# Optimization experiments

Measured on AMD Instinct MI355X. Metric: run time of the kernel, lower is better.

Reference implementation:

```python
import jax, jax.numpy as jnp
import numpy as np

KS = 4          # kernel_size per pseudo-dim (open linear B-splines, degree 1)
GRID = 28       # level-0 grid side
BATCH = 256     # number of graphs
NUM_FIRST_FC = 49


def _grid(n, B):
    """Batched 8-neighborhood grid graph with 2D pseudo-coords in [0,1]."""
    rs, cs = np.meshgrid(np.arange(n), np.arange(n), indexing='ij')
    idx = rs * n + cs
    src_l, dst_l, ps_l = [], [], []
    for dr in (-1, 0, 1):
        for dc in (-1, 0, 1):
            if dr == 0 and dc == 0:
                continue
            r2, c2 = rs + dr, cs + dc
            ok = (r2 >= 0) & (r2 < n) & (c2 >= 0) & (c2 < n)
            src_l.append(idx[ok])
            dst_l.append((r2 * n + c2)[ok])
            m = int(ok.sum())
            ps_l.append(np.stack([np.full(m, (dr + 1) / 2.0),
                                  np.full(m, (dc + 1) / 2.0)], 1))
    src = np.concatenate(src_l)
    dst = np.concatenate(dst_l)
    pseudo = np.concatenate(ps_l).astype(np.float32)
    off = (np.arange(B) * n * n)[:, None]
    src_b = (src[None] + off).reshape(-1)
    dst_b = (dst[None] + off).reshape(-1)
    return (np.stack([src_b, dst_b]).astype(np.int32),
            np.tile(pseudo, (B, 1)))


def _cluster(n, B):
    """Factor-4 (2x2 block) graclus-style cluster assignment, batched."""
    rs, cs = np.meshgrid(np.arange(n), np.arange(n), indexing='ij')
    c = ((rs // 2) * (n // 2) + (cs // 2)).reshape(-1)
    off = (np.arange(B) * (n // 2) ** 2)[:, None]
    return (c[None] + off).reshape(-1).astype(np.int32)


def setup_inputs() -> dict:
    key = jax.random.key(0)
    ks = jax.random.split(key, 16)
    e0, p0 = _grid(GRID, BATCH)          # 28x28 level
    e1, p1 = _grid(GRID // 2, BATCH)     # 14x14 level
    c0 = _cluster(GRID, BATCH)           # 784 -> 196 per graph
    c1 = _cluster(GRID // 2, BATCH)      # 196 -> 49 per graph
    N0 = BATCH * GRID * GRID
    s = 0.1
    inp = {
        'x': jax.random.normal(ks[0], (N0, 1), jnp.float32),
        'edge_index0': jnp.asarray(e0), 'pseudo0': jnp.asarray(p0),
        'edge_index1': jnp.asarray(e1), 'pseudo1': jnp.asarray(p1),
        'cluster0': jnp.asarray(c0), 'cluster1': jnp.asarray(c1),
        'W1': s * jax.random.normal(ks[1], (16, 1, 32), jnp.float32),
        'root1': s * jax.random.normal(ks[2], (1, 32), jnp.float32),
        'b1': jnp.zeros((32,), jnp.float32),
        'W2': s * jax.random.normal(ks[3], (16, 32, 32), jnp.float32),
        'root2': s * jax.random.normal(ks[4], (32, 32), jnp.float32),
        'b2': jnp.zeros((32,), jnp.float32),
        'W3': s * jax.random.normal(ks[5], (16, 32, 64), jnp.float32),
        'root3': s * jax.random.normal(ks[6], (32, 64), jnp.float32),
        'b3': jnp.zeros((64,), jnp.float32),
        'W4': s * jax.random.normal(ks[7], (16, 64, 64), jnp.float32),
        'root4': s * jax.random.normal(ks[8], (64, 64), jnp.float32),
        'b4': jnp.zeros((64,), jnp.float32),
        'fc1_W': s * jax.random.normal(ks[9], (NUM_FIRST_FC * 64, 512), jnp.float32),
        'fc1_b': jnp.zeros((512,), jnp.float32),
        'fc2_W': s * jax.random.normal(ks[10], (512, 10), jnp.float32),
        'fc2_b': jnp.zeros((10,), jnp.float32),
    }
    return inp


def spline_conv(x, src, dst, pseudo, W, root, bias):
    """SplineGCN layer: degree-1 open B-spline weighting over 2D pseudo-coords,
    mean aggregation over incoming edges, plus root weight and bias."""
    n = x.shape[0]
    pos = pseudo * (KS - 1)                       # [E,2] in [0, KS-1]
    i0f = jnp.clip(jnp.floor(pos), 0, KS - 2)
    frac = pos - i0f                              # [E,2]
    i0 = i0f.astype(jnp.int32)
    XW = jnp.einsum('ni,kio->kno', x, W)          # [K, N, out]: per-kernel transform
    msg = jnp.zeros((src.shape[0], W.shape[2]), x.dtype)
    for a in (0, 1):
        wa = frac[:, 0] if a else 1.0 - frac[:, 0]
        for b in (0, 1):
            wb = frac[:, 1] if b else 1.0 - frac[:, 1]
            k = (i0[:, 0] + a) * KS + (i0[:, 1] + b)     # flat kernel index [E]
            msg = msg + (wa * wb)[:, None] * XW[k, src]  # gather per-edge
    agg = jax.ops.segment_sum(msg, dst, num_segments=n)
    deg = jax.ops.segment_sum(jnp.ones_like(dst, dtype=x.dtype), dst,
                              num_segments=n)
    return agg / jnp.maximum(deg, 1.0)[:, None] + x @ root + bias


def pool4(x, cluster):
    # GraclusMaxPool(2): two halving levels == factor-4 cluster max-pool
    return jax.ops.segment_max(x, cluster, num_segments=x.shape[0] // 4)


def reference(x, edge_index0, pseudo0, edge_index1, pseudo1, cluster0, cluster1,
              W1, root1, b1, W2, root2, b2, W3, root3, b3, W4, root4, b4,
              fc1_W, fc1_b, fc2_W, fc2_b):
    s0, d0 = edge_index0[0], edge_index0[1]
    s1, d1 = edge_index1[0], edge_index1[1]
    h = jax.nn.elu(spline_conv(x, s0, d0, pseudo0, W1, root1, b1))
    h = jax.nn.elu(spline_conv(h, s0, d0, pseudo0, W2, root2, b2))
    h = pool4(h, cluster0)
    h = jax.nn.elu(spline_conv(h, s1, d1, pseudo1, W3, root3, b3))
    h = jax.nn.elu(spline_conv(h, s1, d1, pseudo1, W4, root4, b4))
    h = pool4(h, cluster1)
    h = h.reshape(-1, NUM_FIRST_FC * 64)           # [B, 49*64]
    h = jax.nn.elu(h @ fc1_W + fc1_b)
    # dropout is identity in eval / deterministic reference
    logits = h @ fc2_W + fc2_b
    return jax.nn.log_softmax(logits, axis=-1)
```

## Files before the change

kernel.cpp:

```cpp
#include <hip/hip_runtime.h>

typedef unsigned short u16;
typedef short bf16x8 __attribute__((ext_vector_type(8)));
typedef float f32x4 __attribute__((ext_vector_type(4)));

__device__ __constant__ const int DRS[8] = {-1,-1,-1, 0, 0, 1, 1, 1};
__device__ __constant__ const int DCS[8] = {-1, 0, 1,-1, 1,-1, 0, 1};

__device__ inline float bf2f(u16 u) { return __uint_as_float(((unsigned)u) << 16); }
__device__ inline u16 f2bf(float f) {
  unsigned u = __float_as_uint(f);
  return (u16)((u + 0x7fffu + ((u >> 16) & 1u)) >> 16);
}
__device__ inline float eluf(float v) { return v > 0.f ? v : (__expf(v) - 1.f); }
__device__ inline unsigned pk2(float a, float b) {
  return (unsigned)f2bf(a) | ((unsigned)f2bf(b) << 16);
}

__device__ inline float weff_val(const float* __restrict__ W, int d, int off, int stride) {
  int dd = d >= 4 ? d + 1 : d;
  int dr = dd / 3 - 1, dc = dd - (dd / 3) * 3 - 1;
  int kr0, kr1, nr; float wr0, wr1;
  if (dr < 0)       { kr0 = 0; wr0 = 1.f; kr1 = 0; wr1 = 0.f; nr = 1; }
  else if (dr == 0) { kr0 = 1; wr0 = .5f; kr1 = 2; wr1 = .5f; nr = 2; }
  else              { kr0 = 3; wr0 = 1.f; kr1 = 0; wr1 = 0.f; nr = 1; }
  int kc0, kc1, nc; float wc0, wc1;
  if (dc < 0)       { kc0 = 0; wc0 = 1.f; kc1 = 0; wc1 = 0.f; nc = 1; }
  else if (dc == 0) { kc0 = 1; wc0 = .5f; kc1 = 2; wc1 = .5f; nc = 2; }
  else              { kc0 = 3; wc0 = 1.f; kc1 = 0; wc1 = 0.f; nc = 1; }
  float acc = wr0 * wc0 * W[(kr0 * 4 + kc0) * stride + off];
  if (nc == 2) acc += wr0 * wc1 * W[(kr0 * 4 + kc1) * stride + off];
  if (nr == 2) {
    acc += wr1 * wc0 * W[(kr1 * 4 + kc0) * stride + off];
    if (nc == 2) acc += wr1 * wc1 * W[(kr1 * 4 + kc1) * stride + off];
  }
  return acc;
}

__device__ inline int kperm32(int p) { return (p >> 1) + ((p & 1) << 4); }

__global__ __launch_bounds__(256) void pack_all(
    const float* __restrict__ W1,
    const float* __restrict__ W2, const float* __restrict__ rt2,
    const float* __restrict__ W3, const float* __restrict__ rt3,
    const float* __restrict__ W4, const float* __restrict__ rt4,
    const float* __restrict__ fcW,
    float* __restrict__ wf1, u16* __restrict__ wp2,
    u16* __restrict__ wp3, u16* __restrict__ wp4, u16* __restrict__ wfc) {
  __shared__ u16 T[32 * 514];
  int blk = blockIdx.x, t = threadIdx.x;
  if (blk < 98) {
    int q = blk;
#pragma unroll
    for (int i = 0; i < 16; ++i) {
      int idx = i * 1024 + t * 4;
      int k = idx >> 9, n = idx & 511;
      float4 v = *reinterpret_cast<const float4*>(fcW + (size_t)(q * 32 + k) * 512 + n);
      T[k * 514 + n]     = f2bf(v.x);
      T[k * 514 + n + 1] = f2bf(v.y);
      T[k * 514 + n + 2] = f2bf(v.z);
      T[k * 514 + n + 3] = f2bf(v.w);
    }
    __syncthreads();
#pragma unroll
    for (int w = 0; w < 8; ++w) {
      int g = w * 256 + t;
      int nt = g >> 6, l = g & 63;
      union { int4 q4; u16 s[8]; } R;
#pragma unroll
      for (int j = 0; j < 8; ++j)
        R.s[j] = T[((l >> 4) * 8 + j) * 514 + nt * 16 + (l & 15)];
      *reinterpret_cast<int4*>(wfc + ((size_t)(q * 32 + nt) * 64 + l) * 8) = R.q4;
    }
    return;
  }
  int idx = (blk - 98) * 256 + t;
  if (idx < 256) {
    int d = idx >> 5, o = idx & 31;
    wf1[idx] = weff_val(W1, d, o, 32);
    return;
  }
  if (idx < 9472) {
    int local = idx - 256;
    int j = local & 7, l = (local >> 3) & 63, chunk = local >> 9;
    int ct = chunk & 1, tap = chunk >> 1;
    int k = (l >> 4) * 8 + j, n = ct * 16 + (l & 15);
    float v = tap < 8 ? weff_val(W2, tap, k * 32 + n, 1024) : rt2[k * 32 + n];
    wp2[local] = f2bf(v);
    return;
  }
  if (idx < 27904) {
    int local = idx - 9472;
    int j = local & 7, l = (local >> 3) & 63, chunk = local >> 9;
    int ct = chunk & 3, tap = chunk >> 2;
    int k = kperm32((l >> 4) * 8 + j), n = ct * 16 + (l & 15);
    float v = tap < 8 ? weff_val(W3, tap, k * 64 + n, 2048) : rt3[k * 64 + n];
    wp3[local] = f2bf(v);
    return;
  }
  if (idx < 64768) {
    int local = idx - 27904;
    int j = local & 7, l = (local >> 3) & 63, chunk = local >> 9;
    int q = chunk & 1, tmp = chunk >> 1;
    int ct = tmp & 3, tap = tmp >> 2;
    int k = q * 32 + kperm32((l >> 4) * 8 + j), n = ct * 16 + (l & 15);
    float v = tap < 8 ? weff_val(W4, tap, k * 64 + n, 4096) : rt4[k * 64 + n];
    wp4[local] = f2bf(v);
  }
}

__global__ __launch_bounds__(1024, 4) void conv_mega(
    const float* __restrict__ x,
    const float* __restrict__ wf1, const float* __restrict__ rt1, const float* __restrict__ b1,
    const u16* __restrict__ wp2, const float* __restrict__ b2,
    const u16* __restrict__ wp3, const float* __restrict__ b3,
    const u16* __restrict__ wp4, const float* __restrict__ b4,
    u16* __restrict__ A6) {
  extern __shared__ char smem[];
  int4* H1 = (int4*)smem;
  int4* H3 = (int4*)smem;
  u16*  H5 = (u16*)(smem + 17408);
  int4* H4 = (int4*)(smem + 42496);
  unsigned* H4u = (unsigned*)(smem + 42496);
  float* XT = (float*)(smem + 61568);
  int4*     H2 = (int4*)(smem + 75520);
  unsigned* H2u = (unsigned*)(smem + 75520);

  int img = blockIdx.x, tid = threadIdx.x;
  int lane = tid & 63, wid = tid >> 6;
  int kcb = lane >> 4, n0 = lane & 15;
  int4 z4 = make_int4(0, 0, 0, 0);
  f32x4 zz = {0.f, 0.f, 0.f, 0.f};

  for (int i = tid; i < 3848; i += 1024) H1[i] = z4;
  if (tid < 960) {
    int r = tid >> 5, c = tid & 31;
    bool in = (r >= 1) && (r <= 28) && (c >= 1) && (c <= 28);
    XT[tid] = in ? x[(size_t)img * 784 + (r - 1) * 28 + (c - 1)] : 0.f;
  }
  __syncthreads();

  if (tid < 784) {
    int px = tid;
    int r = px / 28, c = px - 28 * (px / 28);
    float acc[32];
#pragma unroll
    for (int o = 0; o < 32; ++o) acc[o] = 0.f;
#pragma unroll
    for (int d = 0; d < 8; ++d) {
      float xv = XT[(r + 1 - DRS[d]) * 32 + (c + 1 - DCS[d])];
#pragma unroll
      for (int o = 0; o < 32; ++o) acc[o] = fmaf(xv, wf1[d * 32 + o], acc[o]);
    }
    float inv = 1.f / (float)((3 - (r == 0) - (r == 27)) * (3 - (c == 0) - (c == 27)) - 1);
    float xc = XT[(r + 1) * 32 + c + 1];
    unsigned pk[16];
#pragma unroll
    for (int h = 0; h < 16; ++h)
      pk[h] = pk2(eluf(acc[2 * h] * inv + xc * rt1[2 * h] + b1[2 * h]),
                  eluf(acc[2 * h + 1] * inv + xc * rt1[2 * h + 1] + b1[2 * h + 1]));
#pragma unroll
    for (int kc = 0; kc < 4; ++kc)
      H1[kc * 962 + (r + 1) * 32 + (c + 1)] =
          make_int4(pk[4 * kc], pk[4 * kc + 1], pk[4 * kc + 2], pk[4 * kc + 3]);
  }
  __syncthreads();

  {
    bf16x8 w2[9][2];
#pragma unroll
    for (int tap = 0; tap < 9; ++tap)
#pragma unroll
      for (int ct = 0; ct < 2; ++ct)
        w2[tap][ct] = *(const bf16x8*)(wp2 + (tap * 2 + ct) * 512 + lane * 8);
    for (int t = wid; t < 49; t += 16) {
      int pxm = t * 16 + n0;
      int r = pxm / 28, c = pxm - 28 * (pxm / 28);
      f32x4 an[2] = {zz, zz}, ar[2] = {zz, zz};
#pragma unroll
      for (int d = 0; d < 8; ++d) {
        bf16x8 a = *(const bf16x8*)&H1[kcb * 962 + (r + 1 - DRS[d]) * 32 + (c + 1 - DCS[d])];
        an[0] = __builtin_amdgcn_mfma_f32_16x16x32_bf16(a, w2[d][0], an[0], 0, 0, 0);
        an[1] = __builtin_amdgcn_mfma_f32_16x16x32_bf16(a, w2[d][1], an[1], 0, 0, 0);
      }
      {
        bf16x8 a = *(const bf16x8*)&H1[kcb * 962 + (r + 1) * 32 + (c + 1)];
        ar[0] = __builtin_amdgcn_mfma_f32_16x16x32_bf16(a, w2[8][0], ar[0], 0, 0, 0);
        ar[1] = __builtin_amdgcn_mfma_f32_16x16x32_bf16(a, w2[8][1], ar[1], 0, 0, 0);
      }
#pragma unroll
      for (int j = 0; j < 4; ++j) {
        int pm = t * 16 + (lane >> 4) * 4 + j;
        int rm = pm / 28, cm = pm - 28 * (pm / 28);
        float inv = 1.f / (float)((3 - (rm == 0) - (rm == 27)) * (3 - (cm == 0) - (cm == 27)) - 1);
        H2u[pm * 16 + n0] = pk2(eluf(an[0][j] * inv + ar[0][j] + b2[n0]),
                                eluf(an[1][j] * inv + ar[1][j] + b2[16 + n0]));
      }
    }
  }
  __syncthreads();

  for (int i = tid; i < 1032; i += 1024) {
    int kc = i & 3, rem = i >> 2;
    int4 v = z4;
    if (rem < 256) {
      int pr = rem >> 4, pc = rem & 15;
      if (pr >= 1 && pr <= 14 && pc >= 1 && pc <= 14) {
        int px0 = (2 * (pr - 1)) * 28 + 2 * (pc - 1);
        union { int4 q; u16 s[8]; } A, B, C, D, R;
        A.q = H2[px0 * 4 + kc]; B.q = H2[(px0 + 1) * 4 + kc];
        C.q = H2[(px0 + 28) * 4 + kc]; D.q = H2[(px0 + 29) * 4 + kc];
#pragma unroll
        for (int e = 0; e < 8; ++e)
          R.s[e] = f2bf(fmaxf(fmaxf(bf2f(A.s[e]), bf2f(B.s[e])),
                              fmaxf(bf2f(C.s[e]), bf2f(D.s[e]))));
        v = R.q;
      }
    }
    H3[kc * 258 + rem] = v;
  }
  for (int i = tid; i < 2064; i += 1024) H4[i] = z4;
  __syncthreads();

  {
    int ct0 = wid & 1, t0 = wid >> 1;
    bf16x8 w3[9][2];
#pragma unroll
    for (int tap = 0; tap < 9; ++tap)
#pragma unroll
      for (int cc = 0; cc < 2; ++cc)
        w3[tap][cc] = *(const bf16x8*)(wp3 + (tap * 4 + ct0 * 2 + cc) * 512 + lane * 8);
    for (int t = t0; t < 13; t += 8) {
      int pxm = t * 16 + n0; if (pxm > 195) pxm = 195;
      int r = pxm / 14, c = pxm - 14 * (pxm / 14);
      f32x4 an[2] = {zz, zz}, ar[2] = {zz, zz};
#pragma unroll
      for (int d = 0; d < 8; ++d) {
        bf16x8 a = *(const bf16x8*)&H3[kcb * 258 + (r + 1 - DRS[d]) * 16 + (c + 1 - DCS[d])];
        an[0] = __builtin_amdgcn_mfma_f32_16x16x32_bf16(a, w3[d][0], an[0], 0, 0, 0);
        an[1] = __builtin_amdgcn_mfma_f32_16x16x32_bf16(a, w3[d][1], an[1], 0, 0, 0);
      }
      {
        bf16x8 a = *(const bf16x8*)&H3[kcb * 258 + (r + 1) * 16 + (c + 1)];
        ar[0] = __builtin_amdgcn_mfma_f32_16x16x32_bf16(a, w3[8][0], ar[0], 0, 0, 0);
        ar[1] = __builtin_amdgcn_mfma_f32_16x16x32_bf16(a, w3[8][1], ar[1], 0, 0, 0);
      }
#pragma unroll
      for (int j = 0; j < 4; ++j) {
        int pm = t * 16 + (lane >> 4) * 4 + j;
        if (pm < 196) {
          int rm = pm / 14, cm = pm - 14 * (pm / 14);
          float inv = 1.f / (float)((3 - (rm == 0) - (rm == 13)) * (3 - (cm == 0) - (cm == 13)) - 1);
          unsigned v = pk2(eluf(an[0][j] * inv + ar[0][j] + b3[ct0 * 32 + n0]),
                           eluf(an[1][j] * inv + ar[1][j] + b3[ct0 * 32 + 16 + n0]));
          H4u[((ct0 * 4 + (n0 >> 2)) * 258 + (rm + 1) * 16 + (cm + 1)) * 4 + (n0 & 3)] = v;
        }
      }
    }
  }
  __syncthreads();

  {
    int ctg = wid & 3, t0 = wid >> 2;
    bf16x8 w4[9][2];
#pragma unroll
    for (int tap = 0; tap < 9; ++tap)
#pragma unroll
      for (int kq = 0; kq < 2; ++kq)
        w4[tap][kq] = *(const bf16x8*)(wp4 + ((tap * 4 + ctg) * 2 + kq) * 512 + lane * 8);
    for (int t = t0; t < 13; t += 4) {
      int pxm = t * 16 + n0; if (pxm > 195) pxm = 195;
      int r = pxm / 14, c = pxm - 14 * (pxm / 14);
      f32x4 an = zz, ar = zz;
#pragma unroll
      for (int d = 0; d < 8; ++d) {
        int rr = r + 1 - DRS[d], c2 = c + 1 - DCS[d];
#pragma unroll
        for (int kq = 0; kq < 2; ++kq) {
          bf16x8 a = *(const bf16x8*)&H4[(kq * 4 + kcb) * 258 + rr * 16 + c2];
          an = __builtin_amdgcn_mfma_f32_16x16x32_bf16(a, w4[d][kq], an, 0, 0, 0);
        }
      }
#pragma unroll
      for (int kq = 0; kq < 2; ++kq) {
        bf16x8 a = *(const bf16x8*)&H4[(kq * 4 + kcb) * 258 + (r + 1) * 16 + (c + 1)];
        ar = __builtin_amdgcn_mfma_f32_16x16x32_bf16(a, w4[8][kq], ar, 0, 0, 0);
      }
#pragma unroll
      for (int j = 0; j < 4; ++j) {
        int pm = t * 16 + (lane >> 4) * 4 + j;
        if (pm < 196) {
          int rm = pm / 14, cm = pm - 14 * (pm / 14);
          float inv = 1.f / (float)((3 - (rm == 0) - (rm == 13)) * (3 - (cm == 0) - (cm == 13)) - 1);
          int n = ctg * 16 + n0;
          H5[pm * 64 + n] = f2bf(eluf(an[j] * inv + ar[j] + b4[n]));
        }
      }
    }
  }
  __syncthreads();

  if (tid < 392) {
    int kc = tid & 7, q = tid >> 3;
    int r2 = q / 7, c2 = q - 7 * (q / 7);
    int px0 = (2 * r2) * 14 + 2 * c2;
    union { int4 q4; u16 s[8]; } A, B, C, D, R;
    A.q4 = *(const int4*)&H5[px0 * 64 + kc * 8];
    B.q4 = *(const int4*)&H5[(px0 + 1) * 64 + kc * 8];
    C.q4 = *(const int4*)&H5[(px0 + 14) * 64 + kc * 8];
    D.q4 = *(const int4*)&H5[(px0 + 15) * 64 + kc * 8];
#pragma unroll
    for (int e = 0; e < 8; ++e)
      R.s[e] = f2bf(fmaxf(fmaxf(bf2f(A.s[e]), bf2f(B.s[e])),
                          fmaxf(bf2f(C.s[e]), bf2f(D.s[e]))));
    *(int4*)(A6 + ((size_t)img * 49 + q) * 64 + kc * 8) = R.q4;
  }
}

__global__ __launch_bounds__(128) void fc1_mfma(
    const u16* __restrict__ A6, const u16* __restrict__ wfc,
    const float* __restrict__ fc1b, u16* __restrict__ h) {
  int blk = blockIdx.x;
  int mt = blk & 15, bn = blk >> 4;
  int lane = threadIdx.x & 63, w = threadIdx.x >> 6;
  int NT = bn * 2 + w;
  f32x4 acc0 = {0.f, 0.f, 0.f, 0.f}, acc1 = {0.f, 0.f, 0.f, 0.f};
  const u16* Ab = A6 + (size_t)(mt * 16 + (lane & 15)) * 3136 + (lane >> 4) * 8;
  const u16* Bb = wfc + (size_t)NT * 512 + (size_t)lane * 8;
#pragma unroll 7
  for (int qq = 0; qq < 98; qq += 2) {
    bf16x8 a0 = *(const bf16x8*)(Ab + qq * 32);
    bf16x8 b0 = *(const bf16x8*)(Bb + (size_t)qq * 16384);
    acc0 = __builtin_amdgcn_mfma_f32_16x16x32_bf16(a0, b0, acc0, 0, 0, 0);
    bf16x8 a1 = *(const bf16x8*)(Ab + qq * 32 + 32);
    bf16x8 b1 = *(const bf16x8*)(Bb + (size_t)qq * 16384 + 16384);
    acc1 = __builtin_amdgcn_mfma_f32_16x16x32_bf16(a1, b1, acc1, 0, 0, 0);
  }
#pragma unroll
  for (int j = 0; j < 4; ++j) {
    int row = mt * 16 + (lane >> 4) * 4 + j;
    int col = NT * 16 + (lane & 15);
    float v = acc0[j] + acc1[j] + fc1b[col];
    h[(size_t)row * 512 + col] = f2bf(eluf(v));
  }
}

__global__ __launch_bounds__(64) void fc2_kernel(
    const u16* __restrict__ h, const float* __restrict__ W,
    const float* __restrict__ bias, float* __restrict__ out) {
  int bb = blockIdx.x;
  int t = threadIdx.x;
  float acc[10];
#pragma unroll
  for (int o = 0; o < 10; ++o) acc[o] = 0.f;
  bf16x8 hv = *(const bf16x8*)(h + (size_t)bb * 512 + t * 8);
#pragma unroll
  for (int kk = 0; kk < 8; ++kk) {
    float xv = bf2f((u16)hv[kk]);
    int k = t * 8 + kk;
#pragma unroll
    for (int o = 0; o < 10; ++o) acc[o] = fmaf(xv, W[k * 10 + o], acc[o]);
  }
#pragma unroll
  for (int o = 0; o < 10; ++o) {
    float v = acc[o];
#pragma unroll
    for (int s = 32; s >= 1; s >>= 1) v += __shfl_xor(v, s);
    acc[o] = v + bias[o];
  }
  float m = acc[0];
#pragma unroll
  for (int o = 1; o < 10; ++o) m = fmaxf(m, acc[o]);
  float sum = 0.f;
#pragma unroll
  for (int o = 0; o < 10; ++o) sum += __expf(acc[o] - m);
  float lse = m + __logf(sum);
  if (t < 10) out[bb * 10 + t] = acc[t] - lse;
}

extern "C" void kernel_launch(void* const* d_in, const int* in_sizes, int n_in,
                              void* d_out, int out_size, void* d_ws, size_t ws_size,
                              hipStream_t stream) {
  const float* x    = (const float*)d_in[0];
  const float* W1   = (const float*)d_in[7];
  const float* r1   = (const float*)d_in[8];
  const float* b1   = (const float*)d_in[9];
  const float* W2   = (const float*)d_in[10];
  const float* r2   = (const float*)d_in[11];
  const float* b2   = (const float*)d_in[12];
  const float* W3   = (const float*)d_in[13];
  const float* r3   = (const float*)d_in[14];
  const float* b3   = (const float*)d_in[15];
  const float* W4   = (const float*)d_in[16];
  const float* r4   = (const float*)d_in[17];
  const float* b4   = (const float*)d_in[18];
  const float* fc1W = (const float*)d_in[19];
  const float* fc1b = (const float*)d_in[20];
  const float* fc2W = (const float*)d_in[21];
  const float* fc2b = (const float*)d_in[22];

  char* wsb = (char*)d_ws;
  float* wf1  = (float*)(wsb + 0);
  u16*   wp2  = (u16*)(wsb + 1024);
  u16*   wp3  = (u16*)(wsb + 19456);
  u16*   wp4  = (u16*)(wsb + 56320);
  u16*   wfc  = (u16*)(wsb + 130048);
  u16*   A6   = (u16*)(wsb + 3341312);
  u16*   hbuf = (u16*)(wsb + 4946944);

  pack_all<<<351, 256, 0, stream>>>(W1, W2, r2, W3, r3, W4, r4, fc1W,
                                    wf1, wp2, wp3, wp4, wfc);

  (void)hipFuncSetAttribute((const void*)conv_mega,
                            hipFuncAttributeMaxDynamicSharedMemorySize, 125696);
  conv_mega<<<256, 1024, 125696, stream>>>(x, wf1, r1, b1, wp2, b2, wp3, b3,
                                           wp4, b4, A6);

  fc1_mfma<<<256, 128, 0, stream>>>(A6, wfc, fc1b, hbuf);
  fc2_kernel<<<256, 64, 0, stream>>>(hbuf, fc2W, fc2b, (float*)d_out);
}
```

Measured before the change: 53.08 us.

## Split fused conv kernel into half-image level-0 kernel and level-1 kernel

Splits the single per-image conv_mega kernel into two launches. convA processes each image's 28x28 level in two 14-row halves, recomputing a one-row halo, and writes the pooled 14x14 features to global memory. convB reads that buffer and runs the level-1 convolutions. The goal is to use 512 smaller blocks with less shared memory, raising occupancy and CU coverage for the heavy level-0 stage. The cost is an extra launch, a global round trip for the pooled activations, and redundant halo computation.

Measured after the change: 56.05 us. +5.6%, slower.

```diff
diff --git a/kernel.cpp b/kernel.cpp
--- a/kernel.cpp
+++ b/kernel.cpp
@@ -109,22 +109,124 @@
   }
 }
 
-__global__ __launch_bounds__(1024, 4) void conv_mega(
+__global__ __launch_bounds__(512, 4) void convA(
     const float* __restrict__ x,
     const float* __restrict__ wf1, const float* __restrict__ rt1, const float* __restrict__ b1,
     const u16* __restrict__ wp2, const float* __restrict__ b2,
+    u16* __restrict__ A3) {
+  extern __shared__ char smem[];
+  int4*     H1  = (int4*)smem;
+  float*    XT  = (float*)(smem + 32896);
+  unsigned* H2u = (unsigned*)(smem + 35200);
+  int4*     H2q = (int4*)(smem + 35200);
+
+  int blk = blockIdx.x, tid = threadIdx.x;
+  int img = blk >> 1, half = blk & 1;
+  int base_r = half * 14;
+  int lane = tid & 63, wid = tid >> 6;
+  int kcb = lane >> 4, n0 = lane & 15;
+  int4 z4 = make_int4(0, 0, 0, 0);
+  f32x4 zz = {0.f, 0.f, 0.f, 0.f};
+
+  for (int i = tid; i < 2056; i += 512) H1[i] = z4;
+  for (int i = tid; i < 576; i += 512) {
+    int r = i >> 5, c = i & 31;
+    int gr = base_r - 2 + r, gc = c - 1;
+    bool in = (gr >= 0) && (gr < 28) && (gc >= 0) && (gc < 28);
+    XT[i] = in ? x[(size_t)img * 784 + gr * 28 + gc] : 0.f;
+  }
+  __syncthreads();
+
+  if (tid < 448) {
+    int lr = tid / 28, c = tid - 28 * (tid / 28);
+    int gr = base_r - 1 + lr;
+    if (gr >= 0 && gr < 28) {
+      float acc[32];
+#pragma unroll
+      for (int o = 0; o < 32; ++o) acc[o] = 0.f;
+#pragma unroll
+      for (int d = 0; d < 8; ++d) {
+        float xv = XT[(lr + 1 - DRS[d]) * 32 + (c + 1 - DCS[d])];
+#pragma unroll
+        for (int o = 0; o < 32; ++o) acc[o] = fmaf(xv, wf1[d * 32 + o], acc[o]);
+      }
+      float inv = 1.f / (float)((3 - (gr == 0) - (gr == 27)) * (3 - (c == 0) - (c == 27)) - 1);
+      float xc = XT[(lr + 1) * 32 + c + 1];
+      unsigned pk[16];
+#pragma unroll
+      for (int h = 0; h < 16; ++h)
+        pk[h] = pk2(eluf(acc[2 * h] * inv + xc * rt1[2 * h] + b1[2 * h]),
+                    eluf(acc[2 * h + 1] * inv + xc * rt1[2 * h + 1] + b1[2 * h + 1]));
+#pragma unroll
+      for (int kc = 0; kc < 4; ++kc)
+        H1[kc * 514 + lr * 32 + (c + 1)] =
+            make_int4(pk[4 * kc], pk[4 * kc + 1], pk[4 * kc + 2], pk[4 * kc + 3]);
+    }
+  }
+  __syncthreads();
+
+  {
+    bf16x8 w2[9][2];
+#pragma unroll
+    for (int tap = 0; tap < 9; ++tap)
+#pragma unroll
+      for (int ct = 0; ct < 2; ++ct)
+        w2[tap][ct] = *(const bf16x8*)(wp2 + (tap * 2 + ct) * 512 + lane * 8);
+    for (int t = wid; t < 25; t += 8) {
+      int pxm = t * 16 + n0; if (pxm > 391) pxm = 391;
+      int lr2 = pxm / 28, c = pxm - 28 * (pxm / 28);
+      f32x4 an[2] = {zz, zz}, ar[2] = {zz, zz};
+#pragma unroll
+      for (int d = 0; d < 8; ++d) {
+        bf16x8 a = *(const bf16x8*)&H1[kcb * 514 + (lr2 + 1 - DRS[d]) * 32 + (c + 1 - DCS[d])];
+        an[0] = __builtin_amdgcn_mfma_f32_16x16x32_bf16(a, w2[d][0], an[0], 0, 0, 0);
+        an[1] = __builtin_amdgcn_mfma_f32_16x16x32_bf16(a, w2[d][1], an[1], 0, 0, 0);
+      }
+      {
+        bf16x8 a = *(const bf16x8*)&H1[kcb * 514 + (lr2 + 1) * 32 + (c + 1)];
+        ar[0] = __builtin_amdgcn_mfma_f32_16x16x32_bf16(a, w2[8][0], ar[0], 0, 0, 0);
+        ar[1] = __builtin_amdgcn_mfma_f32_16x16x32_bf16(a, w2[8][1], ar[1], 0, 0, 0);
+      }
+#pragma unroll
+      for (int j = 0; j < 4; ++j) {
+        int pm = t * 16 + (lane >> 4) * 4 + j;
+        if (pm < 392) {
+          int rmg = base_r + pm / 28, cm = pm - 28 * (pm / 28);
+          float inv = 1.f / (float)((3 - (rmg == 0) - (rmg == 27)) * (3 - (cm == 0) - (cm == 27)) - 1);
+          H2u[pm * 16 + n0] = pk2(eluf(an[0][j] * inv + ar[0][j] + b2[n0]),
+                                  eluf(an[1][j] * inv + ar[1][j] + b2[16 + n0]));
+        }
+      }
+    }
+  }
+  __syncthreads();
+
+  if (tid < 392) {
+    int kc = tid & 3, q = tid >> 2;
+    int orl = q / 14, oc = q - 14 * (q / 14);
+    int p0 = (2 * orl) * 28 + 2 * oc;
+    union { int4 q4; u16 s[8]; } A, B, C, D, R;
+    A.q4 = H2q[p0 * 4 + kc];        B.q4 = H2q[(p0 + 1) * 4 + kc];
+    C.q4 = H2q[(p0 + 28) * 4 + kc]; D.q4 = H2q[(p0 + 29) * 4 + kc];
+#pragma unroll
+    for (int e = 0; e < 8; ++e)
+      R.s[e] = f2bf(fmaxf(fmaxf(bf2f(A.s[e]), bf2f(B.s[e])),
+                          fmaxf(bf2f(C.s[e]), bf2f(D.s[e]))));
+    int qg = (half * 7 + orl) * 14 + oc;
+    *(int4*)(A3 + ((size_t)img * 196 + qg) * 32 + kc * 8) = R.q4;
+  }
+}
+
+__global__ __launch_bounds__(1024, 4) void convB(
+    const u16* __restrict__ A3,
     const u16* __restrict__ wp3, const float* __restrict__ b3,
     const u16* __restrict__ wp4, const float* __restrict__ b4,
     u16* __restrict__ A6) {
   extern __shared__ char smem[];
-  int4* H1 = (int4*)smem;
-  int4* H3 = (int4*)smem;
-  u16*  H5 = (u16*)(smem + 17408);
-  int4* H4 = (int4*)(smem + 42496);
+  int4*     H3  = (int4*)smem;
+  u16*      H5  = (u16*)(smem + 17408);
+  int4*     H4  = (int4*)(smem + 42496);
   unsigned* H4u = (unsigned*)(smem + 42496);
-  float* XT = (float*)(smem + 61568);
-  int4*     H2 = (int4*)(smem + 75520);
-  unsigned* H2u = (unsigned*)(smem + 75520);
 
   int img = blockIdx.x, tid = threadIdx.x;
   int lane = tid & 63, wid = tid >> 6;
@@ -132,92 +234,15 @@
   int4 z4 = make_int4(0, 0, 0, 0);
   f32x4 zz = {0.f, 0.f, 0.f, 0.f};
 
-  for (int i = tid; i < 3848; i += 1024) H1[i] = z4;
-  if (tid < 960) {
-    int r = tid >> 5, c = tid & 31;
-    bool in = (r >= 1) && (r <= 28) && (c >= 1) && (c <= 28);
-    XT[tid] = in ? x[(size_t)img * 784 + (r - 1) * 28 + (c - 1)] : 0.f;
-  }
-  __syncthreads();
-
-  if (tid < 784) {
-    int px = tid;
-    int r = px / 28, c = px - 28 * (px / 28);
-    float acc[32];
-#pragma unroll
-    for (int o = 0; o < 32; ++o) acc[o] = 0.f;
-#pragma unroll
-    for (int d = 0; d < 8; ++d) {
-      float xv = XT[(r + 1 - DRS[d]) * 32 + (c + 1 - DCS[d])];
-#pragma unroll
-      for (int o = 0; o < 32; ++o) acc[o] = fmaf(xv, wf1[d * 32 + o], acc[o]);
-    }
-    float inv = 1.f / (float)((3 - (r == 0) - (r == 27)) * (3 - (c == 0) - (c == 27)) - 1);
-    float xc = XT[(r + 1) * 32 + c + 1];
-    unsigned pk[16];
-#pragma unroll
-    for (int h = 0; h < 16; ++h)
-      pk[h] = pk2(eluf(acc[2 * h] * inv + xc * rt1[2 * h] + b1[2 * h]),
-                  eluf(acc[2 * h + 1] * inv + xc * rt1[2 * h + 1] + b1[2 * h + 1]));
-#pragma unroll
-    for (int kc = 0; kc < 4; ++kc)
-      H1[kc * 962 + (r + 1) * 32 + (c + 1)] =
-          make_int4(pk[4 * kc], pk[4 * kc + 1], pk[4 * kc + 2], pk[4 * kc + 3]);
-  }
-  __syncthreads();
-
-  {
-    bf16x8 w2[9][2];
-#pragma unroll
-    for (int tap = 0; tap < 9; ++tap)
-#pragma unroll
-      for (int ct = 0; ct < 2; ++ct)
-        w2[tap][ct] = *(const bf16x8*)(wp2 + (tap * 2 + ct) * 512 + lane * 8);
-    for (int t = wid; t < 49; t += 16) {
-      int pxm = t * 16 + n0;
-      int r = pxm / 28, c = pxm - 28 * (pxm / 28);
-      f32x4 an[2] = {zz, zz}, ar[2] = {zz, zz};
-#pragma unroll
-      for (int d = 0; d < 8; ++d) {
-        bf16x8 a = *(const bf16x8*)&H1[kcb * 962 + (r + 1 - DRS[d]) * 32 + (c + 1 - DCS[d])];
-        an[0] = __builtin_amdgcn_mfma_f32_16x16x32_bf16(a, w2[d][0], an[0], 0, 0, 0);
-        an[1] = __builtin_amdgcn_mfma_f32_16x16x32_bf16(a, w2[d][1], an[1], 0, 0, 0);
-      }
-      {
-        bf16x8 a = *(const bf16x8*)&H1[kcb * 962 + (r + 1) * 32 + (c + 1)];
-        ar[0] = __builtin_amdgcn_mfma_f32_16x16x32_bf16(a, w2[8][0], ar[0], 0, 0, 0);
-        ar[1] = __builtin_amdgcn_mfma_f32_16x16x32_bf16(a, w2[8][1], ar[1], 0, 0, 0);
-      }
-#pragma unroll
-      for (int j = 0; j < 4; ++j) {
-        int pm = t * 16 + (lane >> 4) * 4 + j;
-        int rm = pm / 28, cm = pm - 28 * (pm / 28);
-        float inv = 1.f / (float)((3 - (rm == 0) - (rm == 27)) * (3 - (cm == 0) - (cm == 27)) - 1);
-        H2u[pm * 16 + n0] = pk2(eluf(an[0][j] * inv + ar[0][j] + b2[n0]),
-                                eluf(an[1][j] * inv + ar[1][j] + b2[16 + n0]));
-      }
-    }
-  }
-  __syncthreads();
-
   for (int i = tid; i < 1032; i += 1024) {
     int kc = i & 3, rem = i >> 2;
     int4 v = z4;
     if (rem < 256) {
       int pr = rem >> 4, pc = rem & 15;
-      if (pr >= 1 && pr <= 14 && pc >= 1 && pc <= 14) {
-        int px0 = (2 * (pr - 1)) * 28 + 2 * (pc - 1);
-        union { int4 q; u16 s[8]; } A, B, C, D, R;
-        A.q = H2[px0 * 4 + kc]; B.q = H2[(px0 + 1) * 4 + kc];
-        C.q = H2[(px0 + 28) * 4 + kc]; D.q = H2[(px0 + 29) * 4 + kc];
-#pragma unroll
-        for (int e = 0; e < 8; ++e)
-          R.s[e] = f2bf(fmaxf(fmaxf(bf2f(A.s[e]), bf2f(B.s[e])),
-                              fmaxf(bf2f(C.s[e]), bf2f(D.s[e]))));
-        v = R.q;
-      }
-    }
-    H3[kc * 258 + rem] = v;
+      if (pr >= 1 && pr <= 14 && pc >= 1 && pc <= 14)
+        v = *(const int4*)(A3 + ((size_t)img * 196 + (pr - 1) * 14 + (pc - 1)) * 32 + kc * 8);
+    }
+    if ((i & 3) == kc) H3[kc * 258 + rem] = v;
   }
   for (int i = tid; i < 2064; i += 1024) H4[i] = z4;
   __syncthreads();
@@ -407,14 +432,16 @@
   u16*   wfc  = (u16*)(wsb + 130048);
   u16*   A6   = (u16*)(wsb + 3341312);
   u16*   hbuf = (u16*)(wsb + 4946944);
+  u16*   A3   = (u16*)(wsb + 5209088);
 
   pack_all<<<351, 256, 0, stream>>>(W1, W2, r2, W3, r3, W4, r4, fc1W,
                                     wf1, wp2, wp3, wp4, wfc);
 
-  (void)hipFuncSetAttribute((const void*)conv_mega,
-                            hipFuncAttributeMaxDynamicSharedMemorySize, 125696);
-  conv_mega<<<256, 1024, 125696, stream>>>(x, wf1, r1, b1, wp2, b2, wp3, b3,
-                                           wp4, b4, A6);
+  convA<<<512, 512, 60288, stream>>>(x, wf1, r1, b1, wp2, b2, A3);
+
+  (void)hipFuncSetAttribute((const void*)convB,
+                            hipFuncAttributeMaxDynamicSharedMemorySize, 75520);
+  convB<<<256, 1024, 75520, stream>>>(A3, wp3, b3, wp4, b4, A6);
 
   fc1_mfma<<<256, 128, 0, stream>>>(A6, wfc, fc1b, hbuf);
   fc2_kernel<<<256, 64, 0, stream>>>(hbuf, fc2W, fc2b, (float*)d_out);
```

## Split fc1 K-reduction across four waves and widen conv4 per-wave output tiles

Applied to the files above, without the earlier changes.

The fc1 kernel now runs 512 threads per block. Each block splits the 98-step K loop into four chunks handled by separate waves, and the partial MFMA accumulators are reduced through shared memory. This raises parallelism and the number of memory loads in flight for the bandwidth-bound weight stream. In the conv4 stage, each wave now computes two 16-column output tiles and loads weights from global memory inside the loop instead of preloading them into registers, which cuts register pressure but adds repeated weight loads.

New measurement: 70.04 us. +31.9%, slower.

```diff
diff --git a/kernel.cpp b/kernel.cpp
--- a/kernel.cpp
+++ b/kernel.cpp
@@ -261,30 +261,30 @@
   __syncthreads();
 
   {
-    int ctg = wid & 3, t0 = wid >> 2;
-    bf16x8 w4[9][2];
-#pragma unroll
-    for (int tap = 0; tap < 9; ++tap)
-#pragma unroll
-      for (int kq = 0; kq < 2; ++kq)
-        w4[tap][kq] = *(const bf16x8*)(wp4 + ((tap * 4 + ctg) * 2 + kq) * 512 + lane * 8);
-    for (int t = t0; t < 13; t += 4) {
+    int ct0 = wid & 1, t0 = wid >> 1;
+    for (int t = t0; t < 13; t += 8) {
       int pxm = t * 16 + n0; if (pxm > 195) pxm = 195;
       int r = pxm / 14, c = pxm - 14 * (pxm / 14);
-      f32x4 an = zz, ar = zz;
+      f32x4 an[2] = {zz, zz}, ar[2] = {zz, zz};
 #pragma unroll
       for (int d = 0; d < 8; ++d) {
         int rr = r + 1 - DRS[d], c2 = c + 1 - DCS[d];
 #pragma unroll
         for (int kq = 0; kq < 2; ++kq) {
           bf16x8 a = *(const bf16x8*)&H4[(kq * 4 + kcb) * 258 + rr * 16 + c2];
-          an = __builtin_amdgcn_mfma_f32_16x16x32_bf16(a, w4[d][kq], an, 0, 0, 0);
+          bf16x8 w0 = *(const bf16x8*)(wp4 + ((size_t)((d * 4 + ct0 * 2) * 2 + kq) * 64 + lane) * 8);
+          bf16x8 w1 = *(const bf16x8*)(wp4 + ((size_t)((d * 4 + ct0 * 2 + 1) * 2 + kq) * 64 + lane) * 8);
+          an[0] = __builtin_amdgcn_mfma_f32_16x16x32_bf16(a, w0, an[0], 0, 0, 0);
+          an[1] = __builtin_amdgcn_mfma_f32_16x16x32_bf16(a, w1, an[1], 0, 0, 0);
         }
       }
 #pragma unroll
       for (int kq = 0; kq < 2; ++kq) {
         bf16x8 a = *(const bf16x8*)&H4[(kq * 4 + kcb) * 258 + (r + 1) * 16 + (c + 1)];
-        ar = __builtin_amdgcn_mfma_f32_16x16x32_bf16(a, w4[8][kq], ar, 0, 0, 0);
+        bf16x8 w0 = *(const bf16x8*)(wp4 + ((size_t)((8 * 4 + ct0 * 2) * 2 + kq) * 64 + lane) * 8);
+        bf16x8 w1 = *(const bf16x8*)(wp4 + ((size_t)((8 * 4 + ct0 * 2 + 1) * 2 + kq) * 64 + lane) * 8);
+        ar[0] = __builtin_amdgcn_mfma_f32_16x16x32_bf16(a, w0, ar[0], 0, 0, 0);
+        ar[1] = __builtin_amdgcn_mfma_f32_16x16x32_bf16(a, w1, ar[1], 0, 0, 0);
       }
 #pragma unroll
       for (int j = 0; j < 4; ++j) {
@@ -292,8 +292,9 @@
         if (pm < 196) {
           int rm = pm / 14, cm = pm - 14 * (pm / 14);
           float inv = 1.f / (float)((3 - (rm == 0) - (rm == 13)) * (3 - (cm == 0) - (cm == 13)) - 1);
-          int n = ctg * 16 + n0;
-          H5[pm * 64 + n] = f2bf(eluf(an[j] * inv + ar[j] + b4[n]));
+          int na = ct0 * 32 + n0, nb = ct0 * 32 + 16 + n0;
+          H5[pm * 64 + na] = f2bf(eluf(an[0][j] * inv + ar[0][j] + b4[na]));
+          H5[pm * 64 + nb] = f2bf(eluf(an[1][j] * inv + ar[1][j] + b4[nb]));
         }
       }
     }
@@ -317,31 +318,41 @@
   }
 }
 
-__global__ __launch_bounds__(128) void fc1_mfma(
+__global__ __launch_bounds__(512) void fc1_mfma(
     const u16* __restrict__ A6, const u16* __restrict__ wfc,
     const float* __restrict__ fc1b, u16* __restrict__ h) {
+  __shared__ f32x4 red[8][64];
   int blk = blockIdx.x;
-  int mt = blk & 15, bn = blk >> 4;
-  int lane = threadIdx.x & 63, w = threadIdx.x >> 6;
-  int NT = bn * 2 + w;
-  f32x4 acc0 = {0.f, 0.f, 0.f, 0.f}, acc1 = {0.f, 0.f, 0.f, 0.f};
+  int mt = blk & 15, nt2 = blk >> 4;
+  int lane = threadIdx.x & 63, wid = threadIdx.x >> 6;
+  int half = wid & 1, ks = wid >> 1;
+  int NT = nt2 * 2 + half;
+  const int q0 = ks * 25 - ((ks >= 3) ? 1 : 0);
+  const int q1 = (ks + 1) * 25 - ((ks >= 2) ? 1 : 0);
+  f32x4 acc = {0.f, 0.f, 0.f, 0.f};
   const u16* Ab = A6 + (size_t)(mt * 16 + (lane & 15)) * 3136 + (lane >> 4) * 8;
-  const u16* Bb = wfc + (size_t)NT * 512 + (size_t)lane * 8;
-#pragma unroll 7
-  for (int qq = 0; qq < 98; qq += 2) {
-    bf16x8 a0 = *(const bf16x8*)(Ab + qq * 32);
-    bf16x8 b0 = *(const bf16x8*)(Bb + (size_t)qq * 16384);
-    acc0 = __builtin_amdgcn_mfma_f32_16x16x32_bf16(a0, b0, acc0, 0, 0, 0);
-    bf16x8 a1 = *(const bf16x8*)(Ab + qq * 32 + 32);
-    bf16x8 b1 = *(const bf16x8*)(Bb + (size_t)qq * 16384 + 16384);
-    acc1 = __builtin_amdgcn_mfma_f32_16x16x32_bf16(a1, b1, acc1, 0, 0, 0);
-  }
-#pragma unroll
-  for (int j = 0; j < 4; ++j) {
-    int row = mt * 16 + (lane >> 4) * 4 + j;
-    int col = NT * 16 + (lane & 15);
-    float v = acc0[j] + acc1[j] + fc1b[col];
-    h[(size_t)row * 512 + col] = f2bf(eluf(v));
+  for (int qq = q0; qq < q1; ++qq) {
+    bf16x8 a = *(const bf16x8*)(Ab + qq * 32);
+    bf16x8 b = *(const bf16x8*)(wfc + ((size_t)(qq * 32 + NT) * 64 + lane) * 8);
+    acc = __builtin_amdgcn_mfma_f32_16x16x32_bf16(a, b, acc, 0, 0, 0);
+  }
+  red[wid][lane] = acc;
+  __syncthreads();
+  if (wid < 2) {
+    f32x4 s = red[wid][lane];
+#pragma unroll
+    for (int k2 = 1; k2 < 4; ++k2) {
+      f32x4 p = red[k2 * 2 + wid][lane];
+#pragma unroll
+      for (int j = 0; j < 4; ++j) s[j] += p[j];
+    }
+    int NTo = nt2 * 2 + wid;
+#pragma unroll
+    for (int j = 0; j < 4; ++j) {
+      int row = mt * 16 + (lane >> 4) * 4 + j;
+      int col = NTo * 16 + (lane & 15);
+      h[(size_t)row * 512 + col] = f2bf(eluf(s[j] + fc1b[col]));
+    }
   }
 }
 
@@ -416,6 +427,6 @@
   conv_mega<<<256, 1024, 125696, stream>>>(x, wf1, r1, b1, wp2, b2, wp3, b3,
                                            wp4, b4, A6);
 
-  fc1_mfma<<<256, 128, 0, stream>>>(A6, wfc, fc1b, hbuf);
+  fc1_mfma<<<256, 512, 0, stream>>>(A6, wfc, fc1b, hbuf);
   fc2_kernel<<<256, 64, 0, stream>>>(hbuf, fc2W, fc2b, (float*)d_out);
 }
```
